# Optimization experiments

Measured on AMD Instinct MI355X. Metric: run time of the kernel, lower is better.

Reference implementation:

```python
import jax, jax.numpy as jnp
import numpy as np

T, B, F = 512, 512, 14
H1, H2 = 32, 64


def setup_inputs() -> dict:
    key = jax.random.key(0)
    ks = jax.random.split(key, 16)
    s1 = 1.0 / np.sqrt(H1)
    s2 = 1.0 / np.sqrt(H2)
    u = lambda k, shape, s: jax.random.uniform(k, shape, jnp.float32, -s, s)
    return {
        "x": jax.random.normal(ks[0], (T, B, F), jnp.float32),
        # LSTM layer 1 (PyTorch gate order i,f,g,o)
        "W_ih1": u(ks[1], (4 * H1, F), s1),
        "W_hh1": u(ks[2], (4 * H1, H1), s1),
        "b_ih1": u(ks[3], (4 * H1,), s1),
        "b_hh1": u(ks[4], (4 * H1,), s1),
        # LSTM layer 2
        "W_ih2": u(ks[5], (4 * H2, H1), s2),
        "W_hh2": u(ks[6], (4 * H2, H2), s2),
        "b_ih2": u(ks[7], (4 * H2,), s2),
        "b_hh2": u(ks[8], (4 * H2,), s2),
        # MLP head
        "W_fc1": u(ks[9], (8, H2), 1.0 / np.sqrt(H2)),
        "b_fc1": u(ks[10], (8,), 1.0 / np.sqrt(H2)),
        "W_fc2": u(ks[11], (8, 8), 1.0 / np.sqrt(8)),
        "b_fc2": u(ks[12], (8,), 1.0 / np.sqrt(8)),
        "W_fc": u(ks[13], (1, 8), 1.0 / np.sqrt(8)),
        "b_fc": u(ks[14], (1,), 1.0 / np.sqrt(8)),
    }


def _gates(g, c):
    # PyTorch LSTM gate order: input, forget, cell(g), output
    i, f, gg, o = jnp.split(g, 4, axis=-1)
    c_new = jax.nn.sigmoid(f) * c + jax.nn.sigmoid(i) * jnp.tanh(gg)
    h_new = jax.nn.sigmoid(o) * jnp.tanh(c_new)
    return h_new, c_new


def reference(x, W_ih1, W_hh1, b_ih1, b_hh1, W_ih2, W_hh2, b_ih2, b_hh2,
              W_fc1, b_fc1, W_fc2, b_fc2, W_fc, b_fc):
    Bv = x.shape[1]
    # Fold the input projection of layer 1 outside the scan (one big GEMM).
    xg = jnp.einsum('tbf,gf->tbg', x, W_ih1) + b_ih1 + b_hh1  # [T,B,4H1]

    def step(carry, xg_t):
        h1, c1, h2 = carry
        h1, c1 = _gates(xg_t + h1 @ W_hh1.T, c1)
        # Layer 2: original code never carries c_t2 -> incoming cell is always 0.
        g2 = h1 @ W_ih2.T + b_ih2 + h2 @ W_hh2.T + b_hh2
        h2, _ = _gates(g2, jnp.zeros((Bv, H2), x.dtype))
        return (h1, c1, h2), None

    init = (jnp.zeros((Bv, H1), x.dtype),
            jnp.zeros((Bv, H1), x.dtype),
            jnp.zeros((Bv, H2), x.dtype))
    (h1, c1, h2), _ = jax.lax.scan(step, init, xg)

    out = jax.nn.relu(h2)
    out = jax.nn.relu(out @ W_fc1.T + b_fc1)
    out = jax.nn.relu(out @ W_fc2.T + b_fc2)
    return out @ W_fc.T + b_fc  # [B,1]
```

## Files before the change

kernel.cpp:

```cpp
#include <hip/hip_runtime.h>
#include <math.h>

#define TT 512
#define BB 512
#define FF 14
#define H1 32
#define H2 64
#define NR 8
#define NBLK (BB / NR)

typedef _Float16 half8   __attribute__((ext_vector_type(8)));
typedef _Float16 half4_t __attribute__((ext_vector_type(4)));
typedef float    float4v __attribute__((ext_vector_type(4)));

typedef __attribute__((address_space(1))) const half4_t g_half4;

#if __has_builtin(__builtin_amdgcn_exp2f)
__device__ __forceinline__ float exp2_(float x) { return __builtin_amdgcn_exp2f(x); }
#else
__device__ __forceinline__ float exp2_(float x) { return exp2f(x); }
#endif
__device__ __forceinline__ float rcpf_(float x) { return __builtin_amdgcn_rcpf(x); }

__device__ __forceinline__ float dpp_ror8_(float v) {
    return __int_as_float(__builtin_amdgcn_update_dpp(
        0, __float_as_int(v), 0x128 , 0xF, 0xF, true));
}

#define K1L 1.4426950408889634f
#define K2L 2.8853901617779268f

__device__ __forceinline__ float4v mfma16(half8 a, half8 b, float4v c) {
    return __builtin_amdgcn_mfma_f32_16x16x32_f16(a, b, c, 0, 0, 0);
}

__device__ __forceinline__ int bfrag_off(int k, int n) {
    const int slab = k >> 5, k5 = k & 31;
    const int dl = n + 16 * ((k5 >> 3) & 3);
    const int dw = (k5 >> 1) & 3;
    return ((slab * 256 + dl * 4 + dw) << 1) | (k5 & 1);
}

__global__ __launch_bounds__(512)
void xg_precompute(const float* __restrict__ x,
                   const float* __restrict__ Wih1,
                   const float* __restrict__ bih1,
                   const float* __restrict__ bhh1,
                   _Float16* __restrict__ xg)
{
    const int t    = blockIdx.x >> 3;
    const int seg  = blockIdx.x & 7;
    const int l    = threadIdx.x;
    const int lane = l & 63;
    const int w    = l >> 6;
    const int n    = lane & 15;
    const int quad = lane >> 4;
    const int u1   = w * 4 + quad;

    float wr[4][FF];
    float bs[4];
    #pragma unroll
    for (int r = 0; r < 4; ++r) {
        const int row = r * 32 + u1;
        #pragma unroll
        for (int f = 0; f < FF; ++f) wr[r][f] = Wih1[row * FF + f];
        bs[r] = bih1[row] + bhh1[row];
    }

    half4_t* og = (half4_t*)xg + (size_t)t * (NBLK * 256);
    #pragma unroll 2
    for (int bi = 0; bi < 8; ++bi) {
        const int blk = seg * 8 + bi;
        const int row = blk * NR + (n & 7);
        const float* xp = x + ((size_t)t * BB + row) * FF;
        float xv[FF];
        #pragma unroll
        for (int e = 0; e < 7; ++e) {
            const float2 v = *(const float2*)(xp + 2 * e);
            xv[2 * e] = v.x; xv[2 * e + 1] = v.y;
        }
        half4_t o16;
        #pragma unroll
        for (int r = 0; r < 4; ++r) {
            float a = bs[r];
            #pragma unroll
            for (int f = 0; f < FF; ++f) a = fmaf(xv[f], wr[r][f], a);
            o16[r] = (_Float16)a;
        }
        if (n < 8) og[blk * 256 + w * 32 + quad * 8 + n] = o16;
    }
}

#define XGOFF(t_) ((size_t)(t_) * (NBLK * 256))

__global__ __launch_bounds__(1024)
__attribute__((amdgpu_waves_per_eu(4, 4)))
void lstm3_v22(
    const _Float16* __restrict__ xg,
    const float* __restrict__ Wih2, const float* __restrict__ Whh1,
    const float* __restrict__ Whh2,
    const float* __restrict__ bih2, const float* __restrict__ bhh2,
    const float* __restrict__ Wfc1, const float* __restrict__ bfc1,
    const float* __restrict__ Wfc2, const float* __restrict__ bfc2,
    const float* __restrict__ Wfc,  const float* __restrict__ bfc,
    float* __restrict__ out)
{
    const int row0 = blockIdx.x * NR;
    const int l    = threadIdx.x;
    const int lane = l & 63;
    const int wv   = l >> 6;
    const int w    = wv & 7;
    const bool isL1 = (wv < 8);
    const int n    = lane & 15;
    const int quad = lane >> 4;
    const int hi   = n >> 3;

    __shared__ __align__(16) unsigned s2f[2][3 * 256];
    __shared__ _Float16 h2plain[NR][H2];
    __shared__ float mlp1[NR][8];
    __shared__ float mlp2[NR][8];

    half8 a2[2][3];
    float4v bias2[2];
    if (!isL1) {
        #pragma unroll
        for (int tt = 0; tt < 2; ++tt) {
            const int T = 2 * w + tt;
            const int m = T * 16 + n;
            const int row = (m & 3) * 64 + (m >> 2);
            #pragma unroll
            for (int s = 0; s < 3; ++s) {
                const int k0 = s * 32 + quad * 8;
                half8 a;
                if (k0 < H1) {
                    #pragma unroll
                    for (int j = 0; j < 8; ++j) a[j] = (_Float16)Wih2[row * H1 + k0 + j];
                } else {
                    #pragma unroll
                    for (int j = 0; j < 8; ++j) a[j] = (_Float16)Whh2[row * H2 + (k0 - H1) + j];
                }
                a2[tt][s] = a;
            }
            const int u = T * 4 + quad;
            #pragma unroll
            for (int r = 0; r < 4; ++r) {
                const int br = r * 64 + u;
                bias2[tt][r] = bih2[br] + bhh2[br];
            }
        }
    }

    half8 a1h;
    if (isL1) {
        const int m = w * 16 + n;
        const int row = (m & 3) * 32 + (m >> 2);
        #pragma unroll
        for (int j = 0; j < 8; ++j)
            a1h[j] = (_Float16)Whh1[row * H1 + quad * 8 + j];
    }

    const int u1    = w * 4 + quad;
    const int offB  = bfrag_off(u1, n);
    const int u2sel = (2 * w + hi) * 4 + quad;
    const int off2n = bfrag_off(32 + u2sel, n & 7);

    const g_half4* xgb = (const g_half4*)((const half4_t*)xg
                        + (size_t)blockIdx.x * 256 + (w * 32 + quad * 8 + (n & 7)));

    float c1r = 0.0f;

    for (int z = l; z < 2 * 3 * 256; z += 1024) ((unsigned*)s2f)[z] = 0u;

    half4_t xg0 = {0,0,0,0}, xgA = {0,0,0,0}, xgB = {0,0,0,0},
            xgC = {0,0,0,0}, xgD = {0,0,0,0};
    if (isL1) {
        xg0 = xgb[XGOFF(0)];
        xgA = xgb[XGOFF(1)];
        xgB = xgb[XGOFF(2)];
        xgC = xgb[XGOFF(3)];
        xgD = xgb[XGOFF(4)];
    }
    __syncthreads();

#define LSTM_STEP(i_, CP_, RP_, XG_) do {                                          \
        if (isL1) {                                                                \
            const half8 tb0 = *(const half8*)(s2f[RP_] + lane * 4);                \
            const half4_t xh = XG_;                                                \
            { int tn_ = (i_) + 4; if (tn_ > TT - 1) tn_ = TT - 1;                  \
              XG_ = xgb[XGOFF(tn_)]; }                                             \
            float4v cin_;                                                          \
            cin_[0] = (float)xh[0]; cin_[1] = (float)xh[1];                        \
            cin_[2] = (float)xh[2]; cin_[3] = (float)xh[3];                        \
            float4v acc1 = mfma16(a1h, tb0, cin_);                                 \
            const float Ei = exp2_(-K1L * acc1[0]);                                \
            const float Ef = exp2_(-K1L * acc1[1]);                                \
            const float Eg = exp2_(-K2L * acc1[2]);                                \
            const float Eo = exp2_(-K1L * acc1[3]);                                \
            const float P  = (1.0f + Ei) * (1.0f + Eg);                            \
            const float pf = 1.0f + Ef;                                            \
            const float cn = fmaf(c1r, P, pf * (1.0f - Eg)) * rcpf_(pf * P);       \
            c1r = cn;                                                              \
            const float Ec = exp2_(-K2L * cn);                                     \
            const float hh = (1.0f - Ec) * rcpf_((1.0f + Eo) * (1.0f + Ec));       \
            ((_Float16*)s2f[CP_])[offB] = (_Float16)hh;                            \
        } else {                                                                   \
            const half8 tb0 = *(const half8*)(s2f[RP_] + lane * 4);                \
            const half8 tb1 = *(const half8*)(s2f[RP_] + 256 + lane * 4);          \
            const half8 tb2 = *(const half8*)(s2f[RP_] + 512 + lane * 4);          \
            float4v p0 = bias2[0];                                                 \
            p0 = mfma16(a2[0][0], tb0, p0);                                        \
            p0 = mfma16(a2[0][1], tb1, p0);                                        \
            p0 = mfma16(a2[0][2], tb2, p0);                                        \
            float4v p1 = bias2[1];                                                 \
            p1 = mfma16(a2[1][0], tb0, p1);                                        \
            p1 = mfma16(a2[1][1], tb1, p1);                                        \
            p1 = mfma16(a2[1][2], tb2, p1);                                        \
            float4v ps;                                                            \
            _Pragma("unroll")                                                      \
            for (int r = 0; r < 4; ++r) {                                          \
                const float sw = dpp_ror8_(p1[r]);                                 \
                ps[r] = hi ? sw : p0[r];                                           \
            }                                                                      \
            const float Ei = exp2_(-K1L * ps[0]);                                  \
            const float Eg = exp2_(-K2L * ps[2]);                                  \
            const float Eo = exp2_(-K1L * ps[3]);                                  \
            const float c2 = (1.0f - Eg) * rcpf_((1.0f + Ei) * (1.0f + Eg));       \
            const float Ec = exp2_(-K2L * c2);                                     \
            const float h  = (1.0f - Ec) * rcpf_((1.0f + Eo) * (1.0f + Ec));       \
            ((_Float16*)s2f[CP_])[off2n] = (_Float16)h;                            \
        }                                                                          \
        asm volatile("s_waitcnt lgkmcnt(0)" ::: "memory");                         \
        __builtin_amdgcn_s_barrier();                                              \
        asm volatile("" ::: "memory");                                             \
    } while (0)

    {
        if (isL1) {
            const float gi = (float)xg0[0], gg = (float)xg0[2], go = (float)xg0[3];
            const float Ei = exp2_(-K1L * gi);
            const float Eg = exp2_(-K2L * gg);
            const float Eo = exp2_(-K1L * go);
            const float cn = (1.0f - Eg) * rcpf_((1.0f + Ei) * (1.0f + Eg));
            c1r = cn;
            const float Ec = exp2_(-K2L * cn);
            const float hh = (1.0f - Ec) * rcpf_((1.0f + Eo) * (1.0f + Ec));
            ((_Float16*)s2f[0])[offB] = (_Float16)hh;
        }
        asm volatile("s_waitcnt lgkmcnt(0)" ::: "memory");
        __builtin_amdgcn_s_barrier();
        asm volatile("" ::: "memory");
    }

    #pragma unroll 1
    for (int ii = 0; ii < 127; ++ii) {
        const int i0 = 4 * ii + 1;
        LSTM_STEP(i0,     1, 0, xgA);
        LSTM_STEP(i0 + 1, 0, 1, xgB);
        LSTM_STEP(i0 + 2, 1, 0, xgC);
        LSTM_STEP(i0 + 3, 0, 1, xgD);
    }
    LSTM_STEP(509, 1, 0, xgA);
    LSTM_STEP(510, 0, 1, xgB);
    LSTM_STEP(511, 1, 0, xgC);

    if (!isL1) {
        const half8 tb0 = *(const half8*)(s2f[1] + lane * 4);
        const half8 tb1 = *(const half8*)(s2f[1] + 256 + lane * 4);
        const half8 tb2 = *(const half8*)(s2f[1] + 512 + lane * 4);
        float4v p0 = bias2[0];
        p0 = mfma16(a2[0][0], tb0, p0);
        p0 = mfma16(a2[0][1], tb1, p0);
        p0 = mfma16(a2[0][2], tb2, p0);
        float4v p1 = bias2[1];
        p1 = mfma16(a2[1][0], tb0, p1);
        p1 = mfma16(a2[1][1], tb1, p1);
        p1 = mfma16(a2[1][2], tb2, p1);
        float4v ps;
        #pragma unroll
        for (int r = 0; r < 4; ++r) {
            const float sw = dpp_ror8_(p1[r]);
            ps[r] = hi ? sw : p0[r];
        }
        const float Ei = exp2_(-K1L * ps[0]);
        const float Eg = exp2_(-K2L * ps[2]);
        const float Eo = exp2_(-K1L * ps[3]);
        const float c2 = (1.0f - Eg) * rcpf_((1.0f + Ei) * (1.0f + Eg));
        const float Ec = exp2_(-K2L * c2);
        const float h  = (1.0f - Ec) * rcpf_((1.0f + Eo) * (1.0f + Ec));
        h2plain[n & 7][u2sel] = (_Float16)h;
    }
    __syncthreads();

    if (l < NR * 8) {
        const int rr = l >> 3, j = l & 7;
        float a = bfc1[j];
        #pragma unroll
        for (int k = 0; k < H2; ++k)
            a = fmaf(fmaxf((float)h2plain[rr][k], 0.0f), Wfc1[j * H2 + k], a);
        mlp1[rr][j] = fmaxf(a, 0.0f);
    }
    __syncthreads();
    if (l < NR * 8) {
        const int rr = l >> 3, j = l & 7;
        float a = bfc2[j];
        #pragma unroll
        for (int k = 0; k < 8; ++k) a = fmaf(mlp1[rr][k], Wfc2[j * 8 + k], a);
        mlp2[rr][j] = fmaxf(a, 0.0f);
    }
    __syncthreads();
    if (l < NR) {
        float a = bfc[0];
        #pragma unroll
        for (int k = 0; k < 8; ++k) a = fmaf(mlp2[l][k], Wfc[k], a);
        out[row0 + l] = a;
    }
#undef LSTM_STEP
}

__device__ __forceinline__ float sigmoidf_(float x) { return rcpf_(1.0f + __expf(-x)); }
__device__ __forceinline__ float tanhf_(float x) {
    float e = __expf(-2.0f * fabsf(x));
    float t = (1.0f - e) * rcpf_(1.0f + e);
    return copysignf(t, x);
}

__global__ __launch_bounds__(512)
__attribute__((amdgpu_waves_per_eu(2, 2)))
void lstm3_kernel(
    const float* __restrict__ x,
    const float* __restrict__ Wih1, const float* __restrict__ Whh1,
    const float* __restrict__ bih1, const float* __restrict__ bhh1,
    const float* __restrict__ Wih2, const float* __restrict__ Whh2,
    const float* __restrict__ bih2, const float* __restrict__ bhh2,
    const float* __restrict__ Wfc1, const float* __restrict__ bfc1,
    const float* __restrict__ Wfc2, const float* __restrict__ bfc2,
    const float* __restrict__ Wfc,  const float* __restrict__ bfc,
    float* __restrict__ out)
{
    const int row0 = blockIdx.x * 16;
    const int l    = threadIdx.x;
    const int lane = l & 63;
    const int w    = l >> 6;
    const int n    = lane & 15;
    const int quad = lane >> 4;

    __shared__ __align__(16) unsigned s2f[2][3 * 256];
    __shared__ _Float16 h2plain[16][H2];
    __shared__ float mlp1[16][8];
    __shared__ float mlp2[16][8];

    half8 a2[2][3];
    float4v bias2[2];
    #pragma unroll
    for (int tt = 0; tt < 2; ++tt) {
        const int T = 2 * w + tt;
        const int m = T * 16 + n;
        const int row = (m & 3) * 64 + (m >> 2);
        #pragma unroll
        for (int s = 0; s < 3; ++s) {
            const int k0 = s * 32 + quad * 8;
            half8 a;
            if (k0 < H1) {
                #pragma unroll
                for (int j = 0; j < 8; ++j) a[j] = (_Float16)Wih2[row * H1 + k0 + j];
            } else {
                #pragma unroll
                for (int j = 0; j < 8; ++j) a[j] = (_Float16)Whh2[row * H2 + (k0 - H1) + j];
            }
            a2[tt][s] = a;
        }
        const int u = T * 4 + quad;
        #pragma unroll
        for (int r = 0; r < 4; ++r) {
            const int br = r * 64 + u;
            bias2[tt][r] = bih2[br] + bhh2[br];
        }
    }

    half8 a1x, a1h;
    float4v bias1;
    {
        const int m = w * 16 + n;
        const int row = (m & 3) * 32 + (m >> 2);
        #pragma unroll
        for (int j = 0; j < 8; ++j) {
            const int k = quad * 8 + j;
            a1x[j] = (_Float16)((k < FF) ? Wih1[row * FF + k] : 0.0f);
            a1h[j] = (_Float16)Whh1[row * H1 + k];
        }
        const int u1_ = w * 4 + quad;
        #pragma unroll
        for (int r = 0; r < 4; ++r) {
            const int br = r * 32 + u1_;
            bias1[r] = bih1[br] + bhh1[br];
        }
    }

    const int u1   = w * 4 + quad;
    const int offB = bfrag_off(u1, n);
    int off2[2];
    #pragma unroll
    for (int tt = 0; tt < 2; ++tt)
        off2[tt] = bfrag_off(32 + (2 * w + tt) * 4 + quad, n);

    const int b1q  = quad & 1;
    const int xrow = (row0 + n) * FF;
    const int xo0 = 8 * b1q;
    const int xo1 = 8 * b1q + 2;
    const int xo2 = 8 * b1q + 4;
    const int xo3 = 6 * b1q + 6;

    float c1r = 0.0f;
    float2 xr0[4], xr1[4];

    for (int z = l; z < 2 * 3 * 256; z += 512) ((unsigned*)s2f)[z] = 0u;

    {
        const float* xp = x + xrow;
        xr0[0] = *(const float2*)(xp + xo0);
        xr0[1] = *(const float2*)(xp + xo1);
        xr0[2] = *(const float2*)(xp + xo2);
        xr0[3] = *(const float2*)(xp + xo3);
        const float* xq = x + BB * FF + xrow;
        xr1[0] = *(const float2*)(xq + xo0);
        xr1[1] = *(const float2*)(xq + xo1);
        xr1[2] = *(const float2*)(xq + xo2);
        xr1[3] = *(const float2*)(xq + xo3);
    }
    __syncthreads();

#define LSTM_STEP_F(i_, CP_, RP_, XR_) do {                                        \
        const half8 tb0 = *(const half8*)(s2f[RP_] + lane * 4);                    \
        const half8 tb1 = *(const half8*)(s2f[RP_] + 256 + lane * 4);              \
        const half8 tb2 = *(const half8*)(s2f[RP_] + 512 + lane * 4);              \
        half8 xb;                                                                  \
        xb[0] = (_Float16)XR_[0].x; xb[1] = (_Float16)XR_[0].y;                    \
        xb[2] = (_Float16)XR_[1].x; xb[3] = (_Float16)XR_[1].y;                    \
        xb[4] = (_Float16)XR_[2].x; xb[5] = (_Float16)XR_[2].y;                    \
        xb[6] = (_Float16)XR_[3].x; xb[7] = (_Float16)XR_[3].y;                    \
        { int tn_ = (i_) + 2; if (tn_ > TT - 1) tn_ = TT - 1;                      \
          const float* xp_ = x + tn_ * (BB * FF) + xrow;                           \
          XR_[0] = *(const float2*)(xp_ + xo0);                                    \
          XR_[1] = *(const float2*)(xp_ + xo1);                                    \
          XR_[2] = *(const float2*)(xp_ + xo2);                                    \
          XR_[3] = *(const float2*)(xp_ + xo3); }                                  \
        float4v acc1 = mfma16(a1x, xb, bias1);                                     \
        acc1 = mfma16(a1h, tb0, acc1);                                             \
        const float cn1 = sigmoidf_(acc1[1]) * c1r                                 \
                        + sigmoidf_(acc1[0]) * tanhf_(acc1[2]);                    \
        c1r = cn1;                                                                 \
        ((_Float16*)s2f[CP_])[offB] = (_Float16)(sigmoidf_(acc1[3]) * tanhf_(cn1));\
        _Pragma("unroll")                                                          \
        for (int tt = 0; tt < 2; ++tt) {                                           \
            float4v acc = bias2[tt];                                               \
            acc = mfma16(a2[tt][0], tb0, acc);                                     \
            acc = mfma16(a2[tt][1], tb1, acc);                                     \
            acc = mfma16(a2[tt][2], tb2, acc);                                     \
            const float cn = sigmoidf_(acc[0]) * tanhf_(acc[2]);                   \
            const float h  = sigmoidf_(acc[3]) * tanhf_(cn);                       \
            ((_Float16*)s2f[CP_])[off2[tt]] = (_Float16)h;                         \
        }                                                                          \
        asm volatile("s_waitcnt lgkmcnt(0)" ::: "memory");                         \
        __builtin_amdgcn_s_barrier();                                              \
        asm volatile("" ::: "memory");                                             \
    } while (0)

    {
        half8 xb;
        xb[0] = (_Float16)xr0[0].x; xb[1] = (_Float16)xr0[0].y;
        xb[2] = (_Float16)xr0[1].x; xb[3] = (_Float16)xr0[1].y;
        xb[4] = (_Float16)xr0[2].x; xb[5] = (_Float16)xr0[2].y;
        xb[6] = (_Float16)xr0[3].x; xb[7] = (_Float16)xr0[3].y;
        {   const float* xp_ = x + 2 * (BB * FF) + xrow;
            xr0[0] = *(const float2*)(xp_ + xo0);
            xr0[1] = *(const float2*)(xp_ + xo1);
            xr0[2] = *(const float2*)(xp_ + xo2);
            xr0[3] = *(const float2*)(xp_ + xo3); }
        float4v acc1 = mfma16(a1x, xb, bias1);
        const float cn1 = sigmoidf_(acc1[0]) * tanhf_(acc1[2]);
        c1r = cn1;
        ((_Float16*)s2f[0])[offB] = (_Float16)(sigmoidf_(acc1[3]) * tanhf_(cn1));
        asm volatile("s_waitcnt lgkmcnt(0)" ::: "memory");
        __builtin_amdgcn_s_barrier();
        asm volatile("" ::: "memory");
    }

    #pragma unroll 1
    for (int ii = 0; ii < 255; ++ii) {
        const int i0 = 2 * ii + 1;
        LSTM_STEP_F(i0,     1, 0, xr1);
        LSTM_STEP_F(i0 + 1, 0, 1, xr0);
    }
    LSTM_STEP_F(511, 1, 0, xr1);

    {
        const half8 tb0 = *(const half8*)(s2f[1] + lane * 4);
        const half8 tb1 = *(const half8*)(s2f[1] + 256 + lane * 4);
        const half8 tb2 = *(const half8*)(s2f[1] + 512 + lane * 4);
        #pragma unroll
        for (int tt = 0; tt < 2; ++tt) {
            float4v acc = bias2[tt];
            acc = mfma16(a2[tt][0], tb0, acc);
            acc = mfma16(a2[tt][1], tb1, acc);
            acc = mfma16(a2[tt][2], tb2, acc);
            const float cn = sigmoidf_(acc[0]) * tanhf_(acc[2]);
            const float h  = sigmoidf_(acc[3]) * tanhf_(cn);
            h2plain[n][(2 * w + tt) * 4 + quad] = (_Float16)h;
        }
        __syncthreads();
    }

    if (l < 16 * 8) {
        const int rr = l >> 3, j = l & 7;
        float a = bfc1[j];
        #pragma unroll
        for (int k = 0; k < H2; ++k)
            a = fmaf(fmaxf((float)h2plain[rr][k], 0.0f), Wfc1[j * H2 + k], a);
        mlp1[rr][j] = fmaxf(a, 0.0f);
    }
    __syncthreads();
    if (l < 16 * 8) {
        const int rr = l >> 3, j = l & 7;
        float a = bfc2[j];
        #pragma unroll
        for (int k = 0; k < 8; ++k) a = fmaf(mlp1[rr][k], Wfc2[j * 8 + k], a);
        mlp2[rr][j] = fmaxf(a, 0.0f);
    }
    __syncthreads();
    if (l < 16) {
        float a = bfc[0];
        #pragma unroll
        for (int k = 0; k < 8; ++k) a = fmaf(mlp2[l][k], Wfc[k], a);
        out[row0 + l] = a;
    }
#undef LSTM_STEP_F
}

extern "C" void kernel_launch(void* const* d_in, const int* in_sizes, int n_in,
                              void* d_out, int out_size, void* d_ws, size_t ws_size,
                              hipStream_t stream) {
    const float* x    = (const float*)d_in[0];
    const float* Wih1 = (const float*)d_in[1];
    const float* Whh1 = (const float*)d_in[2];
    const float* bih1 = (const float*)d_in[3];
    const float* bhh1 = (const float*)d_in[4];
    const float* Wih2 = (const float*)d_in[5];
    const float* Whh2 = (const float*)d_in[6];
    const float* bih2 = (const float*)d_in[7];
    const float* bhh2 = (const float*)d_in[8];
    const float* Wfc1 = (const float*)d_in[9];
    const float* bfc1 = (const float*)d_in[10];
    const float* Wfc2 = (const float*)d_in[11];
    const float* bfc2 = (const float*)d_in[12];
    const float* Wfc  = (const float*)d_in[13];
    const float* bfc  = (const float*)d_in[14];
    float* out = (float*)d_out;

    const size_t xg_bytes = (size_t)TT * NBLK * 256 * sizeof(half4_t);
    if (d_ws != nullptr && ws_size >= xg_bytes) {
        _Float16* xg = (_Float16*)d_ws;
        xg_precompute<<<dim3(TT * 8), dim3(512), 0, stream>>>(x, Wih1, bih1, bhh1, xg);
        lstm3_v22<<<dim3(NBLK), dim3(1024), 0, stream>>>(
            xg, Wih2, Whh1, Whh2, bih2, bhh2,
            Wfc1, bfc1, Wfc2, bfc2, Wfc, bfc, out);
    } else {
        lstm3_kernel<<<dim3(BB / 16), dim3(512), 0, stream>>>(
            x, Wih1, Whh1, bih1, bhh1, Wih2, Whh2, bih2, bhh2,
            Wfc1, bfc1, Wfc2, bfc2, Wfc, bfc, out);
    }
}
```

Before: 344.3 us.

## Pack layer-1 LSTM into 4 waves with dual MFMA tiles, stage x via LDS

Layer 1 now runs on 4 waves instead of 8, each issuing two MFMA tiles and merging their halves with a DPP rotate and select. The block shrinks from 1024 to 768 threads with a matching waves-per-EU hint. This cuts the number of waves taking part in each step's barrier and LDS exchange, at the cost of extra per-wave MFMA and shuffle work on the serial recurrence. Separately, the xg precompute kernel stages its x tile into shared memory with one coalesced load instead of each thread doing strided global reads.

```diff
diff --git a/kernel.cpp b/kernel.cpp
--- a/kernel.cpp
+++ b/kernel.cpp
@@ -57,6 +57,16 @@
     const int quad = lane >> 4;
     const int u1   = w * 4 + quad;
 
+    __shared__ __align__(16) float xs[64 * FF];
+
+    {
+        const float* src = x + ((size_t)t * BB + seg * 64) * FF;
+        if (l < 448) {
+            const float2 v = ((const float2*)src)[l];
+            ((float2*)xs)[l] = v;
+        }
+    }
+
     float wr[4][FF];
     float bs[4];
     #pragma unroll
@@ -66,17 +76,17 @@
         for (int f = 0; f < FF; ++f) wr[r][f] = Wih1[row * FF + f];
         bs[r] = bih1[row] + bhh1[row];
     }
+    __syncthreads();
 
     half4_t* og = (half4_t*)xg + (size_t)t * (NBLK * 256);
     #pragma unroll 2
     for (int bi = 0; bi < 8; ++bi) {
         const int blk = seg * 8 + bi;
-        const int row = blk * NR + (n & 7);
-        const float* xp = x + ((size_t)t * BB + row) * FF;
+        const int rb  = (bi * 8 + (n & 7)) * FF;
         float xv[FF];
         #pragma unroll
         for (int e = 0; e < 7; ++e) {
-            const float2 v = *(const float2*)(xp + 2 * e);
+            const float2 v = *(const float2*)&xs[rb + 2 * e];
             xv[2 * e] = v.x; xv[2 * e + 1] = v.y;
         }
         half4_t o16;
@@ -87,15 +97,15 @@
             for (int f = 0; f < FF; ++f) a = fmaf(xv[f], wr[r][f], a);
             o16[r] = (_Float16)a;
         }
-        if (n < 8) og[blk * 256 + w * 32 + quad * 8 + n] = o16;
+        if (n < 8) og[blk * 256 + u1 * 8 + n] = o16;
     }
 }
 
 #define XGOFF(t_) ((size_t)(t_) * (NBLK * 256))
 
-__global__ __launch_bounds__(1024)
-__attribute__((amdgpu_waves_per_eu(4, 4)))
-void lstm3_v22(
+__global__ __launch_bounds__(768)
+__attribute__((amdgpu_waves_per_eu(3, 3)))
+void lstm3_v23(
     const _Float16* __restrict__ xg,
     const float* __restrict__ Wih2, const float* __restrict__ Whh1,
     const float* __restrict__ Whh2,
@@ -109,8 +119,8 @@
     const int l    = threadIdx.x;
     const int lane = l & 63;
     const int wv   = l >> 6;
-    const int w    = wv & 7;
-    const bool isL1 = (wv < 8);
+    const bool isL1 = (wv < 4);
+    const int w2   = wv - 4;
     const int n    = lane & 15;
     const int quad = lane >> 4;
     const int hi   = n >> 3;
@@ -125,7 +135,7 @@
     if (!isL1) {
         #pragma unroll
         for (int tt = 0; tt < 2; ++tt) {
-            const int T = 2 * w + tt;
+            const int T = 2 * w2 + tt;
             const int m = T * 16 + n;
             const int row = (m & 3) * 64 + (m >> 2);
             #pragma unroll
@@ -150,26 +160,31 @@
         }
     }
 
-    half8 a1h;
+    half8 a1h0, a1h1;
     if (isL1) {
-        const int m = w * 16 + n;
-        const int row = (m & 3) * 32 + (m >> 2);
-        #pragma unroll
-        for (int j = 0; j < 8; ++j)
-            a1h[j] = (_Float16)Whh1[row * H1 + quad * 8 + j];
-    }
-
-    const int u1    = w * 4 + quad;
-    const int offB  = bfrag_off(u1, n);
-    const int u2sel = (2 * w + hi) * 4 + quad;
-    const int off2n = bfrag_off(32 + u2sel, n & 7);
+        #pragma unroll
+        for (int tt = 0; tt < 2; ++tt) {
+            const int m = (2 * wv + tt) * 16 + n;
+            const int row = (m & 3) * 32 + (m >> 2);
+            half8 a;
+            #pragma unroll
+            for (int j = 0; j < 8; ++j)
+                a[j] = (_Float16)Whh1[row * H1 + quad * 8 + j];
+            if (tt == 0) a1h0 = a; else a1h1 = a;
+        }
+    }
+
+    const int u1sel = (2 * wv + hi) * 4 + quad;
+    const int offB  = bfrag_off(u1sel & 31, n & 7);
+    const int u2sel = (2 * w2 + hi) * 4 + quad;
+    const int off2n = bfrag_off(32 + (u2sel & 63), n & 7);
 
     const g_half4* xgb = (const g_half4*)((const half4_t*)xg
-                        + (size_t)blockIdx.x * 256 + (w * 32 + quad * 8 + (n & 7)));
+                        + (size_t)blockIdx.x * 256 + ((u1sel & 31) * 8 + (n & 7)));
 
     float c1r = 0.0f;
 
-    for (int z = l; z < 2 * 3 * 256; z += 1024) ((unsigned*)s2f)[z] = 0u;
+    for (int z = l; z < 2 * 3 * 256; z += 768) ((unsigned*)s2f)[z] = 0u;
 
     half4_t xg0 = {0,0,0,0}, xgA = {0,0,0,0}, xgB = {0,0,0,0},
             xgC = {0,0,0,0}, xgD = {0,0,0,0};
@@ -188,14 +203,23 @@
             const half4_t xh = XG_;                                                \
             { int tn_ = (i_) + 4; if (tn_ > TT - 1) tn_ = TT - 1;                  \
               XG_ = xgb[XGOFF(tn_)]; }                                             \
-            float4v cin_;                                                          \
-            cin_[0] = (float)xh[0]; cin_[1] = (float)xh[1];                        \
-            cin_[2] = (float)xh[2]; cin_[3] = (float)xh[3];                        \
-            float4v acc1 = mfma16(a1h, tb0, cin_);                                 \
-            const float Ei = exp2_(-K1L * acc1[0]);                                \
-            const float Ef = exp2_(-K1L * acc1[1]);                                \
-            const float Eg = exp2_(-K2L * acc1[2]);                                \
-            const float Eo = exp2_(-K1L * acc1[3]);                                \
+            const float4v z4 = {0.0f, 0.0f, 0.0f, 0.0f};                           \
+            float4v p0 = mfma16(a1h0, tb0, z4);                                    \
+            float4v p1 = mfma16(a1h1, tb0, z4);                                    \
+            float4v ps;                                                            \
+            _Pragma("unroll")                                                      \
+            for (int r = 0; r < 4; ++r) {                                          \
+                const float sw = dpp_ror8_(p1[r]);                                 \
+                ps[r] = hi ? sw : p0[r];                                           \
+            }                                                                      \
+            const float g0 = ps[0] + (float)xh[0];                                 \
+            const float g1 = ps[1] + (float)xh[1];                                 \
+            const float g2 = ps[2] + (float)xh[2];                                 \
+            const float g3 = ps[3] + (float)xh[3];                                 \
+            const float Ei = exp2_(-K1L * g0);                                     \
+            const float Ef = exp2_(-K1L * g1);                                     \
+            const float Eg = exp2_(-K2L * g2);                                     \
+            const float Eo = exp2_(-K1L * g3);                                     \
             const float P  = (1.0f + Ei) * (1.0f + Eg);                            \
             const float pf = 1.0f + Ef;                                            \
             const float cn = fmaf(c1r, P, pf * (1.0f - Eg)) * rcpf_(pf * P);       \
@@ -560,7 +584,7 @@
     if (d_ws != nullptr && ws_size >= xg_bytes) {
         _Float16* xg = (_Float16*)d_ws;
         xg_precompute<<<dim3(TT * 8), dim3(512), 0, stream>>>(x, Wih1, bih1, bhh1, xg);
-        lstm3_v22<<<dim3(NBLK), dim3(1024), 0, stream>>>(
+        lstm3_v23<<<dim3(NBLK), dim3(768), 0, stream>>>(
             xg, Wih2, Whh1, Whh2, bih2, bhh2,
             Wfc1, bfc1, Wfc2, bfc2, Wfc, bfc, out);
     } else {
```

New measurement: 297.8 us. 1.16x faster.
